# Optimization experiments

Measured on AMD Instinct MI355X. Metric: run time of the kernel, lower is better.

Reference implementation:

```python
import jax, jax.numpy as jnp
import numpy as np

H = 8      # heads
D = 64     # dim_head
N0 = 1024  # modality-0 tokens
N1 = 1024  # modality-1 tokens
N = N0 + N1  # == token_num
DI = H * D   # dim_inner = 512


def setup_inputs() -> dict:
    key = jax.random.key(0)
    ks = jax.random.split(key, 10)
    s = 0.02
    return {
        "x0": jax.random.normal(ks[0], (1, N0, 512), jnp.float32),
        "x1": jax.random.normal(ks[1], (1, N1, 512), jnp.float32),
        "mask0": jnp.ones((1, N0), jnp.bool_),
        "mask1": jnp.ones((1, N1), jnp.bool_),
        "attn_dist": jax.random.normal(ks[2], (1, N, N), jnp.float32),
        "W_in0": jax.random.normal(ks[3], (512, 3 * DI), jnp.float32) * s,
        "W_in1": jax.random.normal(ks[4], (512, 3 * DI), jnp.float32) * s,
        "W_tau": jax.random.normal(ks[5], (DI, N * H), jnp.float32) * s,
        "b_tau": jax.random.normal(ks[6], (N * H,), jnp.float32) * s,
        "W_out0": jax.random.normal(ks[7], (DI, 512), jnp.float32) * s,
        "W_out1": jax.random.normal(ks[8], (DI, 512), jnp.float32) * s,
    }


def _split_heads(qkv, B, n):
    # (B, n, 3*H*D) -> (3, B, H, n, D)   [matches Rearrange 'b n (qkv h d) -> qkv b h n d']
    return qkv.reshape(B, n, 3, H, D).transpose(2, 0, 3, 1, 4)


def reference(x0, x1, mask0, mask1, attn_dist, W_in0, W_in1, W_tau, b_tau, W_out0, W_out1):
    B = x0.shape[0]
    qkv0 = _split_heads(x0 @ W_in0, B, N0)
    qkv1 = _split_heads(x1 @ W_in1, B, N1)
    qkv = jnp.concatenate([qkv0, qkv1], axis=3)  # pack along token axis -> (3,B,H,N,D)
    q, k, v = qkv[0], qkv[1], qkv[2]
    mask = jnp.concatenate([mask0, mask1], axis=1)  # (B, N)

    sim = jnp.einsum('bhid,bhjd->bhij', q, k) / jnp.sqrt(jnp.array(D, q.dtype))
    neg = -jnp.finfo(sim.dtype).max
    sim = jnp.where(mask[:, None, None, :], sim, neg)

    # taus: raw row-major reshape of q (B,H,N,D) -> (B,N,H*D), as in torch .reshape
    q_flat = q.reshape(B, N, H * D)
    taus = (q_flat @ W_tau + b_tau).reshape(B, N, N, H)
    bias = (taus * attn_dist[..., None]).transpose(0, 3, 1, 2)  # (B,H,N,N)
    sim = sim - bias

    attn = jax.nn.softmax(sim.astype(jnp.float32), axis=-1).astype(sim.dtype)
    out = jnp.einsum('bhij,bhjd->bhid', attn, v)
    out = out.transpose(0, 2, 1, 3).reshape(B, N, H * D)  # merge heads

    out0 = out[:, :N0] @ W_out0
    out1 = out[:, N0:] @ W_out1
    return (out0, out1)
```

## Files before the change

kernel.cpp:

```cpp
#include <hip/hip_runtime.h>
#include <stdint.h>

typedef __bf16 bf16;
typedef __bf16 bf16x8 __attribute__((ext_vector_type(8)));
typedef float f32x4 __attribute__((ext_vector_type(4)));
typedef unsigned short u16x8 __attribute__((ext_vector_type(8)));

#define MFMA16(a, b, c) __builtin_amdgcn_mfma_f32_16x16x32_bf16(a, b, c, 0, 0, 0)

static __device__ __forceinline__ bf16x8 lds_frag(const unsigned short* p) {
  return __builtin_bit_cast(bf16x8, *(const u16x8*)p);
}

static __device__ __forceinline__ bf16x8 gmem_frag(const bf16* p) {
  return __builtin_bit_cast(bf16x8, *(const u16x8*)p);
}

static __device__ __forceinline__ u16x8 cvt8(const float* p) {
  f32x4 a = *(const f32x4*)p;
  f32x4 b = *(const f32x4*)(p + 4);
  u16x8 r;
#pragma unroll
  for (int e = 0; e < 4; ++e) {
    r[e] = __builtin_bit_cast(unsigned short, (bf16)a[e]);
    r[4 + e] = __builtin_bit_cast(unsigned short, (bf16)b[e]);
  }
  return r;
}

__global__ __launch_bounds__(256) void prep_kernel(
    const float* __restrict__ Wti, const float* __restrict__ btau,
    const float* __restrict__ x0, const float* __restrict__ x1,
    const float* __restrict__ Win0, const float* __restrict__ Win1,
    const float* __restrict__ Wo0, const float* __restrict__ Wo1,
    bf16* __restrict__ Wto, float* __restrict__ bto, bf16* __restrict__ xb,
    bf16* __restrict__ Winb0, bf16* __restrict__ Winb1,
    bf16* __restrict__ Wob0, bf16* __restrict__ Wob1) {
  const int b = blockIdx.x;
  const int tid = threadIdx.x;
  __shared__ unsigned short shm[8 * 32 * 72];

  if (b < 512) {
    const int c0 = (b & 7) * 64;
    const int j0 = (b >> 3) * 32;
#pragma unroll
    for (int it = 0; it < 8; ++it) {
      int idx = it * 256 + tid;
      int c = idx >> 5, j = idx & 31;
      u16x8 v = cvt8(Wti + (size_t)(c0 + c) * 16384 + (j0 + j) * 8);
#pragma unroll
      for (int h = 0; h < 8; ++h) shm[(h * 32 + j) * 72 + c] = v[h];
    }
    __syncthreads();
#pragma unroll
    for (int it = 0; it < 8; ++it) {
      int chunk = it * 256 + tid;
      int row = chunk >> 3, ck = chunk & 7;
      int h = row >> 5, j = row & 31;
      u16x8 v = *(const u16x8*)&shm[row * 72 + ck * 8];
      *(u16x8*)((unsigned short*)Wto + (size_t)(h * 2048 + j0 + j) * 512 + c0 + ck * 8) = v;
    }
    if ((b & 7) == 0) {
      int j = tid >> 3, h = tid & 7;
      bto[h * 2048 + j0 + j] = btau[(j0 + j) * 8 + h];
    }
  } else if (b < 896) {
    int t = b - 512;
    const float* W = t < 192 ? Win0 : Win1;
    bf16* Wb = t < 192 ? Winb0 : Winb1;
    t = t < 192 ? t : t - 192;
    const int c0 = (t & 7) * 64, n0 = (t >> 3) * 64;
#pragma unroll
    for (int it = 0; it < 2; ++it) {
      int idx = it * 256 + tid;
      int c = idx >> 3, nn = idx & 7;
      u16x8 v = cvt8(W + (size_t)(c0 + c) * 1536 + n0 + nn * 8);
#pragma unroll
      for (int e = 0; e < 8; ++e) shm[(nn * 8 + e) * 72 + c] = v[e];
    }
    __syncthreads();
#pragma unroll
    for (int it = 0; it < 2; ++it) {
      int idx = it * 256 + tid;
      int n = idx >> 3, ck = idx & 7;
      *(u16x8*)((unsigned short*)Wb + (size_t)(n0 + n) * 512 + c0 + ck * 8) =
          *(const u16x8*)&shm[n * 72 + ck * 8];
    }
  } else if (b < 1408) {
    int t = b - 896;
    const float* src = t < 256 ? x0 : x1;
    size_t dst0 = t < 256 ? 0 : 524288;
    int tt = t < 256 ? t : t - 256;
    size_t off = (size_t)tt * 2048 + tid * 8;
    u16x8 v = cvt8(src + off);
    *(u16x8*)((unsigned short*)xb + dst0 + off) = v;
  } else {
    int t = b - 1408;
    const float* W = t < 64 ? Wo0 : Wo1;
    bf16* Wb = t < 64 ? Wob0 : Wob1;
    t &= 63;
    const int c0 = (t & 7) * 64, n0 = (t >> 3) * 64;
#pragma unroll
    for (int it = 0; it < 2; ++it) {
      int idx = it * 256 + tid;
      int c = idx >> 3, nn = idx & 7;
      u16x8 v = cvt8(W + (size_t)(c0 + c) * 512 + n0 + nn * 8);
#pragma unroll
      for (int e = 0; e < 8; ++e) shm[(nn * 8 + e) * 72 + c] = v[e];
    }
    __syncthreads();
#pragma unroll
    for (int it = 0; it < 2; ++it) {
      int idx = it * 256 + tid;
      int n = idx >> 3, ck = idx & 7;
      *(u16x8*)((unsigned short*)Wb + (size_t)(n0 + n) * 512 + c0 + ck * 8) =
          *(const u16x8*)&shm[n * 72 + ck * 8];
    }
  }
}

__global__ __launch_bounds__(256) void qkv_gemm(
    const bf16* __restrict__ xb, const bf16* __restrict__ Winb0, const bf16* __restrict__ Winb1,
    bf16* __restrict__ Qb, bf16* __restrict__ Kb, bf16* __restrict__ Vt_g) {
  const int i0 = blockIdx.x * 128, c0 = blockIdx.y * 128;
  const bf16* Bm = (i0 < 1024) ? Winb0 : Winb1;
  const int tid = threadIdx.x;
  const int lane = tid & 63, wave = tid >> 6;
  const int l16 = lane & 15, quad = lane >> 4;
  const int mrow = (wave & 1) * 64, ncol = (wave >> 1) * 64;
  __shared__ unsigned short As[128 * 64];
  __shared__ unsigned short Bs[128 * 64];
  f32x4 acc[4][4] = {};

  for (int k0 = 0; k0 < 512; k0 += 64) {
    __syncthreads();
#pragma unroll
    for (int c = 0; c < 4; ++c) {
      int s = c * 256 + tid;
      int row = s >> 3, pos = s & 7;
      int kc = pos ^ (row & 7);
      __builtin_amdgcn_global_load_lds((const unsigned int*)(xb + (size_t)(i0 + row) * 512 + k0 + kc * 8),
                                       (unsigned int*)&As[s * 8], 16, 0, 0);
      __builtin_amdgcn_global_load_lds((const unsigned int*)(Bm + (size_t)(c0 + row) * 512 + k0 + kc * 8),
                                       (unsigned int*)&Bs[s * 8], 16, 0, 0);
    }
    __syncthreads();
#pragma unroll
    for (int kb = 0; kb < 2; ++kb) {
      bf16x8 a[4], b[4];
#pragma unroll
      for (int mt = 0; mt < 4; ++mt) {
        int row = mrow + mt * 16 + l16;
        a[mt] = lds_frag(&As[row * 64 + (((kb * 4 + quad) ^ (row & 7)) * 8)]);
      }
#pragma unroll
      for (int nt = 0; nt < 4; ++nt) {
        int row = ncol + nt * 16 + l16;
        b[nt] = lds_frag(&Bs[row * 64 + (((kb * 4 + quad) ^ (row & 7)) * 8)]);
      }
#pragma unroll
      for (int mt = 0; mt < 4; ++mt)
#pragma unroll
        for (int nt = 0; nt < 4; ++nt) acc[mt][nt] = MFMA16(a[mt], b[nt], acc[mt][nt]);
    }
  }
#pragma unroll
  for (int mt = 0; mt < 4; ++mt)
#pragma unroll
    for (int nt = 0; nt < 4; ++nt)
#pragma unroll
      for (int r = 0; r < 4; ++r) {
        int row = i0 + mrow + mt * 16 + quad * 4 + r;
        int col = c0 + ncol + nt * 16 + l16;
        int qsel = col >> 9, h = (col >> 6) & 7, d = col & 63;
        bf16 val = (bf16)acc[mt][nt][r];
        if (qsel == 2) {
          Vt_g[(size_t)(h * 64 + d) * 2048 + row] = val;
        } else {
          bf16* dst = qsel == 0 ? Qb : Kb;
          dst[(size_t)(h * 2048 + row) * 64 + d] = val;
        }
      }
}

__global__ __launch_bounds__(256) void tau_gemm(
    const bf16* __restrict__ Qb, const bf16* __restrict__ Wt,
    const float* __restrict__ bt, const float* __restrict__ ad, bf16* __restrict__ T) {
  const int i0 = blockIdx.x * 128;
  const int j0 = blockIdx.y * 16;
  const int tid = threadIdx.x;
  const int lane = tid & 63, wave = tid >> 6;
  const int l16 = lane & 15, quad = lane >> 4;
  const int mrow = (wave & 1) * 64, ncol = (wave >> 1) * 64;
  __shared__ unsigned short As[128 * 128];
  __shared__ unsigned short Bs[128 * 128];
  f32x4 acc[4][4] = {};

  for (int k0 = 0; k0 < 512; k0 += 128) {
    __syncthreads();
#pragma unroll
    for (int c = 0; c < 8; ++c) {
      int s = c * 256 + tid;
      int row = s >> 4, pos = s & 15;
      int kc = pos ^ (row & 7);
      __builtin_amdgcn_global_load_lds((const unsigned int*)(Qb + (size_t)(i0 + row) * 512 + k0 + kc * 8),
                                       (unsigned int*)&As[s * 8], 16, 0, 0);
      __builtin_amdgcn_global_load_lds(
          (const unsigned int*)(Wt + (size_t)((row >> 4) * 2048 + j0 + (row & 15)) * 512 + k0 + kc * 8),
          (unsigned int*)&Bs[s * 8], 16, 0, 0);
    }
    __syncthreads();
#pragma unroll
    for (int kb = 0; kb < 4; ++kb) {
      bf16x8 a[4], b[4];
#pragma unroll
      for (int mt = 0; mt < 4; ++mt) {
        int row = mrow + mt * 16 + l16;
        a[mt] = lds_frag(&As[row * 128 + (((kb * 4 + quad) ^ (row & 7)) * 8)]);
      }
#pragma unroll
      for (int nt = 0; nt < 4; ++nt) {
        int row = ncol + nt * 16 + l16;
        b[nt] = lds_frag(&Bs[row * 128 + (((kb * 4 + quad) ^ (row & 7)) * 8)]);
      }
#pragma unroll
      for (int mt = 0; mt < 4; ++mt)
#pragma unroll
        for (int nt = 0; nt < 4; ++nt) acc[mt][nt] = MFMA16(a[mt], b[nt], acc[mt][nt]);
    }
  }
  float btv[4];
  int hh[4];
#pragma unroll
  for (int nt = 0; nt < 4; ++nt) {
    int c = ncol + nt * 16 + l16;
    hh[nt] = c >> 4;
    btv[nt] = bt[hh[nt] * 2048 + j0 + l16];
  }
#pragma unroll
  for (int mt = 0; mt < 4; ++mt)
#pragma unroll
    for (int r = 0; r < 4; ++r) {
      int row = i0 + mrow + mt * 16 + quad * 4 + r;
      float av = ad[(size_t)row * 2048 + j0 + l16];
#pragma unroll
      for (int nt = 0; nt < 4; ++nt)
        T[(size_t)hh[nt] * 4194304 + (size_t)row * 2048 + j0 + l16] =
            (bf16)((acc[mt][nt][r] + btv[nt]) * av);
    }
}

__global__ __launch_bounds__(256) void attn_kernel(
    const bf16* __restrict__ Qb, const bf16* __restrict__ Kb, const bf16* __restrict__ Vt_g,
    const bf16* __restrict__ T, float* __restrict__ Op, float* __restrict__ Ml) {
  const int h = blockIdx.y;
  const int i0 = blockIdx.x * 64;
  const int js = blockIdx.z;
  const int tid = threadIdx.x;
  const int lane = tid & 63, wave = tid >> 6;
  const int l16 = lane & 15, quad = lane >> 4;
  __shared__ unsigned short Ks[64 * 64];
  __shared__ unsigned short Vt[64 * 64];
  __shared__ unsigned short Tb[64 * 64];
  __shared__ unsigned short Ps[64 * 72];

  const bf16* Kh = Kb + (size_t)h * (2048 * 64);
  const bf16* Vh = Vt_g + (size_t)h * (64 * 2048);
  const bf16* Th = T + (size_t)h * (2048 * 2048);

  bf16x8 aQ[2];
#pragma unroll
  for (int kk = 0; kk < 2; ++kk)
    aQ[kk] = gmem_frag(Qb + (size_t)(h * 2048 + i0 + wave * 16 + l16) * 64 + kk * 32 + quad * 8);
  f32x4 Oacc[4] = {};
  float m_run[4], l_run[4];
#pragma unroll
  for (int r = 0; r < 4; ++r) { m_run[r] = -3.0e38f; l_run[r] = 0.f; }
  const int rowl = wave * 16 + quad * 4;

  for (int t = 0; t < 8; ++t) {
    const int j0 = js * 512 + t * 64;
    __syncthreads();
#pragma unroll
    for (int c = 0; c < 2; ++c) {
      int s = c * 256 + tid;
      int r8 = s >> 3, pos = s & 7;
      int sc = pos ^ (r8 & 7);
      __builtin_amdgcn_global_load_lds(
          (const unsigned int*)(Kh + (size_t)(j0 + r8) * 64 + sc * 8),
          (unsigned int*)&Ks[s * 8], 16, 0, 0);
      __builtin_amdgcn_global_load_lds(
          (const unsigned int*)(Vh + (size_t)r8 * 2048 + j0 + sc * 8),
          (unsigned int*)&Vt[s * 8], 16, 0, 0);
      __builtin_amdgcn_global_load_lds(
          (const unsigned int*)(Th + (size_t)(i0 + r8) * 2048 + j0 + pos * 8),
          (unsigned int*)&Tb[s * 8], 16, 0, 0);
    }
    __syncthreads();

    f32x4 S[4] = {};
#pragma unroll
    for (int nt = 0; nt < 4; ++nt) {
      int row = nt * 16 + l16;
#pragma unroll
      for (int kk = 0; kk < 2; ++kk) {
        bf16x8 bk = lds_frag(&Ks[row * 64 + (((kk * 4 + quad) ^ (row & 7)) * 8)]);
        S[nt] = MFMA16(aQ[kk], bk, S[nt]);
      }
    }
    float sv[4][4];
#pragma unroll
    for (int nt = 0; nt < 4; ++nt)
#pragma unroll
      for (int r = 0; r < 4; ++r) {
        float tb = (float)__builtin_bit_cast(bf16, Tb[(rowl + r) * 64 + nt * 16 + l16]);
        sv[nt][r] = S[nt][r] * 0.125f - tb;
      }
#pragma unroll
    for (int r = 0; r < 4; ++r) {
      float mx = fmaxf(fmaxf(sv[0][r], sv[1][r]), fmaxf(sv[2][r], sv[3][r]));
#pragma unroll
      for (int o = 1; o < 16; o <<= 1) mx = fmaxf(mx, __shfl_xor(mx, o, 16));
      float mnew = fmaxf(m_run[r], mx);
      float alpha = __expf(m_run[r] - mnew);
      m_run[r] = mnew;
      float rs = 0.f;
#pragma unroll
      for (int nt = 0; nt < 4; ++nt) { sv[nt][r] = __expf(sv[nt][r] - mnew); rs += sv[nt][r]; }
#pragma unroll
      for (int o = 1; o < 16; o <<= 1) rs += __shfl_xor(rs, o, 16);
      l_run[r] = l_run[r] * alpha + rs;
#pragma unroll
      for (int dt = 0; dt < 4; ++dt) Oacc[dt][r] *= alpha;
    }
#pragma unroll
    for (int nt = 0; nt < 4; ++nt)
#pragma unroll
      for (int r = 0; r < 4; ++r)
        Ps[(rowl + r) * 72 + nt * 16 + l16] =
            __builtin_bit_cast(unsigned short, (bf16)sv[nt][r]);
    __builtin_amdgcn_s_waitcnt(0xC07F);
    __builtin_amdgcn_wave_barrier();
#pragma unroll
    for (int kk = 0; kk < 2; ++kk) {
      bf16x8 aP = lds_frag(&Ps[(wave * 16 + l16) * 72 + kk * 32 + quad * 8]);
#pragma unroll
      for (int dt = 0; dt < 4; ++dt) {
        int row = dt * 16 + l16;
        bf16x8 bv = lds_frag(&Vt[row * 64 + (((kk * 4 + quad) ^ (row & 7)) * 8)]);
        Oacc[dt] = MFMA16(aP, bv, Oacc[dt]);
      }
    }
    __builtin_amdgcn_wave_barrier();
  }
  const size_t pb = ((size_t)js * 8 + h) * 2048;
#pragma unroll
  for (int r = 0; r < 4; ++r) {
    int rowg = i0 + rowl + r;
#pragma unroll
    for (int dt = 0; dt < 4; ++dt)
      Op[(pb + rowg) * 64 + dt * 16 + l16] = Oacc[dt][r];
    if (l16 == 0) {
      Ml[(pb + rowg) * 2 + 0] = m_run[r];
      Ml[(pb + rowg) * 2 + 1] = l_run[r];
    }
  }
}

__global__ __launch_bounds__(256) void merge_kernel(
    const float* __restrict__ Op, const float* __restrict__ Ml, bf16* __restrict__ om) {
  const int gr = blockIdx.x * 4 + (threadIdx.x >> 6);
  const int d = threadIdx.x & 63;
  float ms[4];
  float mmax = -3.0e38f;
#pragma unroll
  for (int s = 0; s < 4; ++s) {
    ms[s] = Ml[((size_t)s * 16384 + gr) * 2 + 0];
    mmax = fmaxf(mmax, ms[s]);
  }
  float lsum = 0.f, o = 0.f;
#pragma unroll
  for (int s = 0; s < 4; ++s) {
    float w = __expf(ms[s] - mmax);
    lsum += Ml[((size_t)s * 16384 + gr) * 2 + 1] * w;
    o += Op[((size_t)s * 16384 + gr) * 64 + d] * w;
  }
  int h = gr >> 11, i = gr & 2047;
  om[(size_t)i * 512 + h * 64 + d] = (bf16)(o / lsum);
}

__global__ __launch_bounds__(256) void out_proj(
    const bf16* __restrict__ om, const bf16* __restrict__ Wob0, const bf16* __restrict__ Wob1,
    float* __restrict__ out) {
  const int mod = blockIdx.z;
  const bf16* Bw = mod ? Wob1 : Wob0;
  float* outp = out + (size_t)mod * (1024 * 512);
  const int i0 = blockIdx.x * 64, c0 = blockIdx.y * 64;
  const int grow0 = mod * 1024 + i0;
  const int tid = threadIdx.x;
  const int lane = tid & 63, wave = tid >> 6;
  const int l16 = lane & 15, quad = lane >> 4;
  const int mrow = (wave & 1) * 32, ncol = (wave >> 1) * 32;
  __shared__ unsigned short As[64 * 64];
  __shared__ unsigned short Bs[64 * 64];
  f32x4 acc[2][2] = {};

  for (int k0 = 0; k0 < 512; k0 += 64) {
    __syncthreads();
#pragma unroll
    for (int c = 0; c < 2; ++c) {
      int s = c * 256 + tid;
      int row = s >> 3, pos = s & 7;
      int kc = pos ^ (row & 7);
      __builtin_amdgcn_global_load_lds((const unsigned int*)(om + (size_t)(grow0 + row) * 512 + k0 + kc * 8),
                                       (unsigned int*)&As[s * 8], 16, 0, 0);
      __builtin_amdgcn_global_load_lds((const unsigned int*)(Bw + (size_t)(c0 + row) * 512 + k0 + kc * 8),
                                       (unsigned int*)&Bs[s * 8], 16, 0, 0);
    }
    __syncthreads();
#pragma unroll
    for (int kb = 0; kb < 2; ++kb) {
      bf16x8 a[2], b[2];
#pragma unroll
      for (int mt = 0; mt < 2; ++mt) {
        int row = mrow + mt * 16 + l16;
        a[mt] = lds_frag(&As[row * 64 + (((kb * 4 + quad) ^ (row & 7)) * 8)]);
      }
#pragma unroll
      for (int nt = 0; nt < 2; ++nt) {
        int row = ncol + nt * 16 + l16;
        b[nt] = lds_frag(&Bs[row * 64 + (((kb * 4 + quad) ^ (row & 7)) * 8)]);
      }
#pragma unroll
      for (int mt = 0; mt < 2; ++mt)
#pragma unroll
        for (int nt = 0; nt < 2; ++nt) acc[mt][nt] = MFMA16(a[mt], b[nt], acc[mt][nt]);
    }
  }
#pragma unroll
  for (int mt = 0; mt < 2; ++mt)
#pragma unroll
    for (int nt = 0; nt < 2; ++nt)
#pragma unroll
      for (int r = 0; r < 4; ++r) {
        int row = i0 + mrow + mt * 16 + quad * 4 + r;
        int col = c0 + ncol + nt * 16 + l16;
        outp[(size_t)row * 512 + col] = acc[mt][nt][r];
      }
}

extern "C" void kernel_launch(void* const* d_in, const int* in_sizes, int n_in,
                              void* d_out, int out_size, void* d_ws, size_t ws_size,
                              hipStream_t stream) {
  (void)in_sizes; (void)n_in; (void)out_size; (void)ws_size;
  const float* x0   = (const float*)d_in[0];
  const float* x1   = (const float*)d_in[1];
  const float* ad   = (const float*)d_in[4];
  const float* Win0 = (const float*)d_in[5];
  const float* Win1 = (const float*)d_in[6];
  const float* Wtau = (const float*)d_in[7];
  const float* btau = (const float*)d_in[8];
  const float* Wo0  = (const float*)d_in[9];
  const float* Wo1  = (const float*)d_in[10];
  float* out = (float*)d_out;

  bf16* ws = (bf16*)d_ws;
  bf16* Qb = ws;
  bf16* Kb = Qb + 1048576;
  bf16* Vt_g = Kb + 1048576;
  bf16* Wt = Vt_g + 1048576;
  bf16* T  = Wt + 8388608;
  bf16* om = T + 33554432;
  float* bt = (float*)(om + 1048576);
  float* Ml = bt + 16384;
  bf16* Wob0 = (bf16*)(Ml + 131072);
  bf16* Wob1 = Wob0 + 262144;
  float* Op = (float*)Wt;
  bf16* xb    = T;
  bf16* Winb0 = T + 1048576;
  bf16* Winb1 = Winb0 + 786432;

  prep_kernel<<<1536, 256, 0, stream>>>(Wtau, btau, x0, x1, Win0, Win1, Wo0, Wo1,
                                        Wt, bt, xb, Winb0, Winb1, Wob0, Wob1);
  qkv_gemm<<<dim3(16, 12), 256, 0, stream>>>(xb, Winb0, Winb1, Qb, Kb, Vt_g);
  tau_gemm<<<dim3(16, 128), 256, 0, stream>>>(Qb, Wt, bt, ad, T);
  attn_kernel<<<dim3(32, 8, 4), 256, 0, stream>>>(Qb, Kb, Vt_g, T, Op, Ml);
  merge_kernel<<<4096, 256, 0, stream>>>(Op, Ml, om);
  out_proj<<<dim3(16, 8, 2), 256, 0, stream>>>(om, Wob0, Wob1, out);
}
```

Measured before the change: 231.2 us.

## Fuse tau bias GEMM into attention kernel, dropping the materialized bias tensor

Removes the separate tau_gemm kernel that wrote a full H×N×N bf16 bias tensor (64 MB) to global memory. The attention kernel now computes each 64x64 bias tile on the fly from the Q row fragments held in registers and streamed tiles of the tau weights, then applies the bias and attn_dist scaling in-register. This trades the round trip of the bias tensor through memory for recomputation inside attention, adds register pressure (16 extra Q fragments per lane), and re-reads the tau weights and attn_dist once per head and query block. The grid is also linearized with head as the fastest-varying index.

```diff
diff --git a/kernel.cpp b/kernel.cpp
--- a/kernel.cpp
+++ b/kernel.cpp
@@ -183,95 +183,38 @@
       }
 }
 
-__global__ __launch_bounds__(256) void tau_gemm(
-    const bf16* __restrict__ Qb, const bf16* __restrict__ Wt,
-    const float* __restrict__ bt, const float* __restrict__ ad, bf16* __restrict__ T) {
-  const int i0 = blockIdx.x * 128;
-  const int j0 = blockIdx.y * 16;
+__global__ __launch_bounds__(256) void fused_attn(
+    const bf16* __restrict__ Qb, const bf16* __restrict__ Kb, const bf16* __restrict__ Vt_g,
+    const bf16* __restrict__ Wt, const float* __restrict__ bt, const float* __restrict__ ad,
+    float* __restrict__ Op, float* __restrict__ Ml) {
+  const int lin = blockIdx.x;
+  const int h = lin & 7;
+  const int m = lin >> 3;
+  const int i0 = (m & 31) * 64;
+  const int js = m >> 5;
   const int tid = threadIdx.x;
   const int lane = tid & 63, wave = tid >> 6;
   const int l16 = lane & 15, quad = lane >> 4;
-  const int mrow = (wave & 1) * 64, ncol = (wave >> 1) * 64;
-  __shared__ unsigned short As[128 * 128];
-  __shared__ unsigned short Bs[128 * 128];
-  f32x4 acc[4][4] = {};
-
-  for (int k0 = 0; k0 < 512; k0 += 128) {
-    __syncthreads();
-#pragma unroll
-    for (int c = 0; c < 8; ++c) {
-      int s = c * 256 + tid;
-      int row = s >> 4, pos = s & 15;
-      int kc = pos ^ (row & 7);
-      __builtin_amdgcn_global_load_lds((const unsigned int*)(Qb + (size_t)(i0 + row) * 512 + k0 + kc * 8),
-                                       (unsigned int*)&As[s * 8], 16, 0, 0);
-      __builtin_amdgcn_global_load_lds(
-          (const unsigned int*)(Wt + (size_t)((row >> 4) * 2048 + j0 + (row & 15)) * 512 + k0 + kc * 8),
-          (unsigned int*)&Bs[s * 8], 16, 0, 0);
-    }
-    __syncthreads();
-#pragma unroll
-    for (int kb = 0; kb < 4; ++kb) {
-      bf16x8 a[4], b[4];
-#pragma unroll
-      for (int mt = 0; mt < 4; ++mt) {
-        int row = mrow + mt * 16 + l16;
-        a[mt] = lds_frag(&As[row * 128 + (((kb * 4 + quad) ^ (row & 7)) * 8)]);
-      }
-#pragma unroll
-      for (int nt = 0; nt < 4; ++nt) {
-        int row = ncol + nt * 16 + l16;
-        b[nt] = lds_frag(&Bs[row * 128 + (((kb * 4 + quad) ^ (row & 7)) * 8)]);
-      }
-#pragma unroll
-      for (int mt = 0; mt < 4; ++mt)
-#pragma unroll
-        for (int nt = 0; nt < 4; ++nt) acc[mt][nt] = MFMA16(a[mt], b[nt], acc[mt][nt]);
-    }
-  }
-  float btv[4];
-  int hh[4];
-#pragma unroll
-  for (int nt = 0; nt < 4; ++nt) {
-    int c = ncol + nt * 16 + l16;
-    hh[nt] = c >> 4;
-    btv[nt] = bt[hh[nt] * 2048 + j0 + l16];
-  }
-#pragma unroll
-  for (int mt = 0; mt < 4; ++mt)
-#pragma unroll
-    for (int r = 0; r < 4; ++r) {
-      int row = i0 + mrow + mt * 16 + quad * 4 + r;
-      float av = ad[(size_t)row * 2048 + j0 + l16];
-#pragma unroll
-      for (int nt = 0; nt < 4; ++nt)
-        T[(size_t)hh[nt] * 4194304 + (size_t)row * 2048 + j0 + l16] =
-            (bf16)((acc[mt][nt][r] + btv[nt]) * av);
-    }
-}
-
-__global__ __launch_bounds__(256) void attn_kernel(
-    const bf16* __restrict__ Qb, const bf16* __restrict__ Kb, const bf16* __restrict__ Vt_g,
-    const bf16* __restrict__ T, float* __restrict__ Op, float* __restrict__ Ml) {
-  const int h = blockIdx.y;
-  const int i0 = blockIdx.x * 64;
-  const int js = blockIdx.z;
-  const int tid = threadIdx.x;
-  const int lane = tid & 63, wave = tid >> 6;
-  const int l16 = lane & 15, quad = lane >> 4;
+  __shared__ unsigned short Ws[64 * 128];
   __shared__ unsigned short Ks[64 * 64];
   __shared__ unsigned short Vt[64 * 64];
-  __shared__ unsigned short Tb[64 * 64];
   __shared__ unsigned short Ps[64 * 72];
 
   const bf16* Kh = Kb + (size_t)h * (2048 * 64);
   const bf16* Vh = Vt_g + (size_t)h * (64 * 2048);
-  const bf16* Th = T + (size_t)h * (2048 * 2048);
-
+  const bf16* Wh = Wt + (size_t)h * (2048 * 512);
+
+  bf16x8 aQt[16];
+  {
+    const bf16* qrow = Qb + (size_t)(i0 + wave * 16 + l16) * 512;
+#pragma unroll
+    for (int kc = 0; kc < 16; ++kc) aQt[kc] = gmem_frag(qrow + kc * 32 + quad * 8);
+  }
   bf16x8 aQ[2];
 #pragma unroll
   for (int kk = 0; kk < 2; ++kk)
     aQ[kk] = gmem_frag(Qb + (size_t)(h * 2048 + i0 + wave * 16 + l16) * 64 + kk * 32 + quad * 8);
+
   f32x4 Oacc[4] = {};
   float m_run[4], l_run[4];
 #pragma unroll
@@ -280,23 +223,47 @@
 
   for (int t = 0; t < 8; ++t) {
     const int j0 = js * 512 + t * 64;
-    __syncthreads();
-#pragma unroll
-    for (int c = 0; c < 2; ++c) {
-      int s = c * 256 + tid;
-      int r8 = s >> 3, pos = s & 7;
-      int sc = pos ^ (r8 & 7);
-      __builtin_amdgcn_global_load_lds(
-          (const unsigned int*)(Kh + (size_t)(j0 + r8) * 64 + sc * 8),
-          (unsigned int*)&Ks[s * 8], 16, 0, 0);
-      __builtin_amdgcn_global_load_lds(
-          (const unsigned int*)(Vh + (size_t)r8 * 2048 + j0 + sc * 8),
-          (unsigned int*)&Vt[s * 8], 16, 0, 0);
-      __builtin_amdgcn_global_load_lds(
-          (const unsigned int*)(Th + (size_t)(i0 + r8) * 2048 + j0 + pos * 8),
-          (unsigned int*)&Tb[s * 8], 16, 0, 0);
-    }
-    __syncthreads();
+    f32x4 acc[4] = {};
+
+#pragma unroll
+    for (int kc4 = 0; kc4 < 4; ++kc4) {
+      __syncthreads();
+      if (kc4 == 0) {
+#pragma unroll
+        for (int c = 0; c < 2; ++c) {
+          int s = c * 256 + tid;
+          int r8 = s >> 3, pos = s & 7;
+          int sc = pos ^ (r8 & 7);
+          __builtin_amdgcn_global_load_lds(
+              (const unsigned int*)(Kh + (size_t)(j0 + r8) * 64 + sc * 8),
+              (unsigned int*)&Ks[s * 8], 16, 0, 0);
+          __builtin_amdgcn_global_load_lds(
+              (const unsigned int*)(Vh + (size_t)r8 * 2048 + j0 + sc * 8),
+              (unsigned int*)&Vt[s * 8], 16, 0, 0);
+        }
+      }
+#pragma unroll
+      for (int c = 0; c < 4; ++c) {
+        int s = c * 256 + tid;
+        int row = s >> 4, pos = s & 15;
+        int kc = pos ^ (row & 7);
+        __builtin_amdgcn_global_load_lds(
+            (const unsigned int*)(Wh + (size_t)(j0 + row) * 512 + kc4 * 128 + kc * 8),
+            (unsigned int*)&Ws[s * 8], 16, 0, 0);
+      }
+      __syncthreads();
+#pragma unroll
+      for (int kb = 0; kb < 4; ++kb) {
+        bf16x8 b[4];
+#pragma unroll
+        for (int nt = 0; nt < 4; ++nt) {
+          int row = nt * 16 + l16;
+          b[nt] = lds_frag(&Ws[row * 128 + (((kb * 4 + quad) ^ (row & 7)) * 8)]);
+        }
+#pragma unroll
+        for (int nt = 0; nt < 4; ++nt) acc[nt] = MFMA16(aQt[kc4 * 4 + kb], b[nt], acc[nt]);
+      }
+    }
 
     f32x4 S[4] = {};
 #pragma unroll
@@ -308,12 +275,16 @@
         S[nt] = MFMA16(aQ[kk], bk, S[nt]);
       }
     }
+    float btv[4];
+#pragma unroll
+    for (int nt = 0; nt < 4; ++nt) btv[nt] = bt[h * 2048 + j0 + nt * 16 + l16];
     float sv[4][4];
 #pragma unroll
     for (int nt = 0; nt < 4; ++nt)
 #pragma unroll
       for (int r = 0; r < 4; ++r) {
-        float tb = (float)__builtin_bit_cast(bf16, Tb[(rowl + r) * 64 + nt * 16 + l16]);
+        float av = ad[(size_t)(i0 + rowl + r) * 2048 + j0 + nt * 16 + l16];
+        float tb = (float)(bf16)((acc[nt][r] + btv[nt]) * av);
         sv[nt][r] = S[nt][r] * 0.125f - tb;
       }
 #pragma unroll
@@ -475,16 +446,15 @@
   float* Ml = bt + 16384;
   bf16* Wob0 = (bf16*)(Ml + 131072);
   bf16* Wob1 = Wob0 + 262144;
-  float* Op = (float*)Wt;
   bf16* xb    = T;
   bf16* Winb0 = T + 1048576;
   bf16* Winb1 = Winb0 + 786432;
+  float* Op   = (float*)T;
 
   prep_kernel<<<1536, 256, 0, stream>>>(Wtau, btau, x0, x1, Win0, Win1, Wo0, Wo1,
                                         Wt, bt, xb, Winb0, Winb1, Wob0, Wob1);
   qkv_gemm<<<dim3(16, 12), 256, 0, stream>>>(xb, Winb0, Winb1, Qb, Kb, Vt_g);
-  tau_gemm<<<dim3(16, 128), 256, 0, stream>>>(Qb, Wt, bt, ad, T);
-  attn_kernel<<<dim3(32, 8, 4), 256, 0, stream>>>(Qb, Kb, Vt_g, T, Op, Ml);
+  fused_attn<<<1024, 256, 0, stream>>>(Qb, Kb, Vt_g, Wt, bt, ad, Op, Ml);
   merge_kernel<<<4096, 256, 0, stream>>>(Op, Ml, om);
   out_proj<<<dim3(16, 8, 2), 256, 0, stream>>>(om, Wob0, Wob1, out);
 }
```

Result: slower. 283.2 us (+22.5%).
